# Kernel optimization log

Measured on AMD Instinct MI355X. Metric: run time of the kernel, lower is better.

Reference implementation:

```python
import jax, jax.numpy as jnp
import numpy as np

N_NODES = 50000
N_EDGES = 640000
D = 128
N_RELS = 16
N_NTYPES = 8


def setup_inputs() -> dict:
    key = jax.random.key(0)
    ks = jax.random.split(key, 9)
    return {
        "feats": jax.random.normal(ks[0], (N_NODES, D), dtype=jnp.float32),
        "W_edge": jax.random.normal(ks[1], (N_RELS, D, D), dtype=jnp.float32) / np.sqrt(D),
        "b_edge": jax.random.normal(ks[2], (N_RELS, D), dtype=jnp.float32) * 0.02,
        "W_node": jax.random.normal(ks[3], (N_NTYPES, D, D), dtype=jnp.float32) / np.sqrt(D),
        "b_node": jax.random.normal(ks[4], (N_NTYPES, D), dtype=jnp.float32) * 0.02,
        "src": jax.random.randint(ks[5], (N_EDGES,), 0, N_NODES, dtype=jnp.int32),
        "dst": jax.random.randint(ks[6], (N_EDGES,), 0, N_NODES, dtype=jnp.int32),
        "ntypes": jax.random.randint(ks[7], (N_NODES,), 0, N_NTYPES, dtype=jnp.int32),
        "etypes": jax.random.randint(ks[8], (N_EDGES,), 0, N_RELS, dtype=jnp.int32),
    }


def reference(feats, W_edge, b_edge, W_node, b_node, src, dst, ntypes, etypes):
    N, d = feats.shape
    T = W_edge.shape[0]
    # Per-relation linear applied to all nodes once: [T, N, out]; then gather per edge.
    hW = jnp.einsum('nd,tdf->tnf', feats, W_edge) + b_edge[:, None, :]
    msg = hW[etypes, src]  # [E, out]
    # Per-(dst-node, edge-type) in-degree counts (one_hot count normalization).
    seg = dst * T + etypes  # [E]
    counts = jax.ops.segment_sum(jnp.ones(msg.shape[0], dtype=msg.dtype), seg,
                                 num_segments=N * T)  # [N*T]
    msg = msg / counts[seg][:, None]
    # Scatter-sum messages into destination nodes (zero for isolated nodes).
    agg = jax.ops.segment_sum(msg, dst, num_segments=N)  # [N, out]
    # Type-conditional node transform + residual message + activation.
    hN = jnp.einsum('nd,tdf->tnf', feats, W_node) + b_node[:, None, :]  # [Tn, N, out]
    out = hN[ntypes, jnp.arange(N)] + agg
    return jax.nn.relu(out)
```

## Files before the change

### kernel.cpp

```cpp
#include <hip/hip_runtime.h>
#include <hip/hip_bf16.h>
#include <stdint.h>


#define D 128
#define TRELS 16
#define NTYPES 8

typedef __bf16 bf16x8 __attribute__((ext_vector_type(8)));
typedef float f32x4 __attribute__((ext_vector_type(4)));

__device__ __forceinline__ unsigned short f2bf(float f) {
  union { float f; unsigned u; } v; v.f = f;
  unsigned u = v.u;
  return (unsigned short)((u + 0x7FFFu + ((u >> 16) & 1u)) >> 16);
}
__device__ __forceinline__ float bf2f(unsigned short h) {
  union { unsigned u; float f; } v; v.u = ((unsigned)h) << 16;
  return v.f;
}

__global__ void prep_k(const float* __restrict__ feats,
                       const float* __restrict__ We,
                       const float* __restrict__ Wn,
                       unsigned short* __restrict__ featsbf,
                       unsigned short* __restrict__ WeT,
                       unsigned short* __restrict__ WnT,
                       int nfeat) {
  int idx = blockIdx.x * 256 + threadIdx.x;
  if (idx < nfeat) { featsbf[idx] = f2bf(feats[idx]); return; }
  idx -= nfeat;
  if (idx < TRELS * D * D) {
    int t = idx >> 14, rem = idx & 16383;
    int n = rem >> 7, k = rem & 127;
    WeT[idx] = f2bf(We[t * 16384 + k * 128 + n]);
    return;
  }
  idx -= TRELS * D * D;
  if (idx < NTYPES * D * D) {
    int t = idx >> 14, rem = idx & 16383;
    int n = rem >> 7, k = rem & 127;
    WnT[idx] = f2bf(Wn[t * 16384 + k * 128 + n]);
  }
}

__global__ void hist_k(const int* __restrict__ dst, const int* __restrict__ etypes,
                       const int* __restrict__ ntypes, int E, int N,
                       int* __restrict__ cnt, int* __restrict__ nhist) {
  __shared__ int sh_n[NTYPES];
  int tid = threadIdx.x;
  if (tid < NTYPES) sh_n[tid] = 0;
  __syncthreads();
  int g = blockIdx.x * 256 + tid;
  if (g < E) atomicAdd(&cnt[dst[g] * TRELS + etypes[g]], 1);
  if (g < N) atomicAdd(&sh_n[ntypes[g]], 1);
  __syncthreads();
  if (tid < NTYPES && sh_n[tid]) atomicAdd(&nhist[tid], sh_n[tid]);
}

__global__ void scan1_k(const int* __restrict__ cnt, int* __restrict__ doff,
                        int* __restrict__ bsum, int N) {
  __shared__ int sd[256];
  int b = blockIdx.x, tid = threadIdx.x;
  int base = b * 1024 + tid * 4;
  int v[4]; int tot = 0;
  for (int j = 0; j < 4; ++j) {
    int i = base + j;
    int dg = 0;
    if (i < N) {
      const int* row = cnt + i * TRELS;
#pragma unroll
      for (int et = 0; et < TRELS; ++et) dg += row[et];
    }
    v[j] = tot; tot += dg;
  }
  sd[tid] = tot;
  __syncthreads();
  for (int off = 1; off < 256; off <<= 1) {
    int t = (tid >= off) ? sd[tid - off] : 0;
    __syncthreads();
    sd[tid] += t;
    __syncthreads();
  }
  int excl = sd[tid] - tot;
  for (int j = 0; j < 4; ++j) {
    int i = base + j;
    if (i < N) doff[i] = excl + v[j];
  }
  if (tid == 255) bsum[b] = sd[255];
}

__global__ void scan2_k(int* __restrict__ misc, int* __restrict__ bsum, int nb) {
  if (threadIdx.x != 0) return;
  int run = 0;
  for (int b = 0; b < nb; ++b) { int t = bsum[b]; bsum[b] = run; run += t; }
  int* noff = misc; int* ntb = misc + 9; int* ncur = misc + 18; int* nhist = misc + 26;
  int s = 0, ts = 0;
  for (int t = 0; t < NTYPES; ++t) {
    noff[t] = s; ncur[t] = s; ntb[t] = ts;
    s += nhist[t]; ts += (nhist[t] + 127) >> 7;
  }
  noff[NTYPES] = s; ntb[NTYPES] = ts;
}

__global__ void scan3_k(int* __restrict__ doff, int* __restrict__ dcur,
                        const int* __restrict__ bsum, int N, int E) {
  int b = blockIdx.x, tid = threadIdx.x;
  int add = bsum[b];
  int base = b * 1024 + tid * 4;
  for (int j = 0; j < 4; ++j) {
    int i = base + j;
    if (i < N) { int o = doff[i] + add; doff[i] = o; dcur[i] = o; }
  }
  if (b == 0 && tid == 0) doff[N] = E;
}

__global__ void scatter_k(const int* __restrict__ src, const int* __restrict__ dst,
                          const int* __restrict__ etypes, const int* __restrict__ ntypes,
                          int E, int N, int* __restrict__ misc,
                          int* __restrict__ dcur,
                          int* __restrict__ edst, int* __restrict__ nsorted) {
  __shared__ int lc_n[NTYPES], lb_n[NTYPES];
  int tid = threadIdx.x;
  if (tid < NTYPES) lc_n[tid] = 0;
  __syncthreads();
  int g = blockIdx.x * 256 + tid;
  if (g < E) {
    int d = dst[g];
    int pos = atomicAdd(&dcur[d], 1);
    edst[pos] = src[g] * TRELS + etypes[g];
  }
  int tn = -1, idn = 0;
  if (g < N) { tn = ntypes[g]; idn = atomicAdd(&lc_n[tn], 1); }
  __syncthreads();
  if (tid < NTYPES && lc_n[tid]) lb_n[tid] = atomicAdd(&misc[18 + tid], lc_n[tid]);
  __syncthreads();
  if (g < N) nsorted[lb_n[tn] + idn] = g;
}

__global__ __launch_bounds__(256) void hw_gemm_k(
    const unsigned short* __restrict__ featsbf,
    const unsigned short* __restrict__ WeT,
    unsigned short* __restrict__ hW, int N) {
  __shared__ unsigned char Asm[128 * 264];
  int tid = threadIdx.x;
  int et = blockIdx.y;
  int tile = blockIdx.x;

  int lane = tid & 63, w = tid >> 6;
  int m = lane & 15, q = lane >> 4;
  int rw = (w & 1) * 64, cw = (w >> 1) * 64;

  const unsigned short* WB = WeT + et * (D * D);
  bf16x8 bfr[4][4];
#pragma unroll
  for (int ks = 0; ks < 4; ++ks)
#pragma unroll
    for (int j = 0; j < 4; ++j)
      bfr[ks][j] = *reinterpret_cast<const bf16x8*>(WB + (cw + j * 16 + m) * D + ks * 32 + q * 8);

  int r = tid >> 1, h = tid & 1;
  int row = tile * 128 + r;
  if (row < N) {
    const uint4* gp = reinterpret_cast<const uint4*>(featsbf + (size_t)row * D);
#pragma unroll
    for (int cc = 0; cc < 8; ++cc) {
      int c = h * 8 + cc;
      *reinterpret_cast<uint4*>(&Asm[r * 256 + ((c ^ (r & 7)) << 4)]) = gp[c];
    }
  }
  __syncthreads();

  f32x4 acc[4][4];
#pragma unroll
  for (int i = 0; i < 4; ++i)
#pragma unroll
    for (int j = 0; j < 4; ++j) acc[i][j] = (f32x4){0.f, 0.f, 0.f, 0.f};

#pragma unroll
  for (int ks = 0; ks < 4; ++ks) {
    bf16x8 a[4];
#pragma unroll
    for (int i = 0; i < 4; ++i) {
      int rr = rw + i * 16 + m;
      int c = ks * 4 + q;
      a[i] = *reinterpret_cast<const bf16x8*>(&Asm[rr * 256 + ((c ^ (rr & 7)) << 4)]);
    }
#pragma unroll
    for (int i = 0; i < 4; ++i)
#pragma unroll
      for (int j = 0; j < 4; ++j)
        acc[i][j] = __builtin_amdgcn_mfma_f32_16x16x32_bf16(a[i], bfr[ks][j], acc[i][j], 0, 0, 0);
  }

  __syncthreads();
  unsigned short* Cs = reinterpret_cast<unsigned short*>(Asm);
#pragma unroll
  for (int i = 0; i < 4; ++i)
#pragma unroll
    for (int j = 0; j < 4; ++j)
#pragma unroll
      for (int reg = 0; reg < 4; ++reg) {
        int rr = rw + i * 16 + q * 4 + reg;
        Cs[rr * 132 + cw + j * 16 + m] = f2bf(acc[i][j][reg]);
      }
  __syncthreads();
  char* gout = (char*)(hW + ((size_t)et * N + (size_t)tile * 128) * D);
#pragma unroll
  for (int cp = 0; cp < 8; ++cp) {
    int o = cp * 4096 + tid * 16;
    int rloc = o >> 8;
    if (tile * 128 + rloc < N) {
      uint4 v = *reinterpret_cast<const uint4*>(&Asm[rloc * 264 + (o & 255)]);
      *reinterpret_cast<uint4*>(gout + o) = v;
    }
  }
}

__global__ __launch_bounds__(256) void agg_k(
    const unsigned short* __restrict__ hW,
    const float* __restrict__ b_edge,
    const int* __restrict__ cnt,
    const int* __restrict__ doff, const int* __restrict__ edst,
    float* __restrict__ agg, int N) {
  int tid = threadIdx.x;
  int lane = tid & 63, w = tid >> 6;
  int d = blockIdx.x * 4 + w;
  if (d >= N) return;

  int cv = 0;
  if (lane < TRELS) cv = cnt[d * TRELS + lane];
  float invl = (cv > 0) ? 1.0f / (float)cv : 0.0f;

  int start = doff[d], end = doff[d + 1];
  float ax = 0.f, ay = 0.f;
  for (int base = start; base < end; base += 64) {
    int key = 0;
    if (base + lane < end) key = edst[base + lane];
    int nchunk = end - base; if (nchunk > 64) nchunk = 64;
    int j = 0;
    for (; j + 4 <= nchunk; j += 4) {
      int k0 = __shfl(key, j, 64), k1 = __shfl(key, j + 1, 64);
      int k2 = __shfl(key, j + 2, 64), k3 = __shfl(key, j + 3, 64);
      float i0 = __shfl(invl, k0 & 15, 64), i1 = __shfl(invl, k1 & 15, 64);
      float i2 = __shfl(invl, k2 & 15, 64), i3 = __shfl(invl, k3 & 15, 64);
      ushort2 h0 = *reinterpret_cast<const ushort2*>(hW + ((size_t)(k0 & 15) * N + (k0 >> 4)) * D + lane * 2);
      ushort2 h1 = *reinterpret_cast<const ushort2*>(hW + ((size_t)(k1 & 15) * N + (k1 >> 4)) * D + lane * 2);
      ushort2 h2 = *reinterpret_cast<const ushort2*>(hW + ((size_t)(k2 & 15) * N + (k2 >> 4)) * D + lane * 2);
      ushort2 h3 = *reinterpret_cast<const ushort2*>(hW + ((size_t)(k3 & 15) * N + (k3 >> 4)) * D + lane * 2);
      ax += i0 * bf2f(h0.x); ay += i0 * bf2f(h0.y);
      ax += i1 * bf2f(h1.x); ay += i1 * bf2f(h1.y);
      ax += i2 * bf2f(h2.x); ay += i2 * bf2f(h2.y);
      ax += i3 * bf2f(h3.x); ay += i3 * bf2f(h3.y);
    }
    for (; j < nchunk; ++j) {
      int k = __shfl(key, j, 64);
      float inv = __shfl(invl, k & 15, 64);
      ushort2 hv = *reinterpret_cast<const ushort2*>(hW + ((size_t)(k & 15) * N + (k >> 4)) * D + lane * 2);
      ax += inv * bf2f(hv.x); ay += inv * bf2f(hv.y);
    }
  }
#pragma unroll
  for (int et = 0; et < TRELS; ++et) {
    int c = __shfl(cv, et, 64);
    if (c > 0) {
      const float* bp = b_edge + et * D + lane * 2;
      ax += bp[0]; ay += bp[1];
    }
  }
  float2* op = reinterpret_cast<float2*>(agg + (size_t)d * D + lane * 2);
  *op = make_float2(ax, ay);
}

__global__ __launch_bounds__(256) void node_gemm_k(
    const unsigned short* __restrict__ featsbf,
    const unsigned short* __restrict__ WnT,
    const float* __restrict__ b_node,
    const int* __restrict__ nsorted, const int* __restrict__ misc,
    const float* __restrict__ agg,
    float* __restrict__ out) {
  __shared__ unsigned char Asm[128 * 264];
  __shared__ int sm_node[128];
  __shared__ int s_ntb[9];
  int tid = threadIdx.x;
  if (tid < 9) s_ntb[tid] = misc[9 + tid];
  __syncthreads();
  int bid = blockIdx.x;
  if (bid >= s_ntb[8]) return;
  int t = 0;
  while (bid >= s_ntb[t + 1]) ++t;
  int tile = bid - s_ntb[t];
  int noff_t = misc[t];
  int cntT = misc[t + 1] - noff_t;

  int lane = tid & 63, w = tid >> 6;
  int m = lane & 15, q = lane >> 4;
  int rw = (w & 1) * 64, cw = (w >> 1) * 64;

  const unsigned short* WB = WnT + t * (D * D);
  bf16x8 bfr[4][4];
#pragma unroll
  for (int ks = 0; ks < 4; ++ks)
#pragma unroll
    for (int j = 0; j < 4; ++j)
      bfr[ks][j] = *reinterpret_cast<const bf16x8*>(WB + (cw + j * 16 + m) * D + ks * 32 + q * 8);

  int r = tid >> 1, h = tid & 1;
  int gidx = tile * 128 + r;
  bool rv = gidx < cntT;
  int node = 0;
  if (rv) node = nsorted[noff_t + gidx];
  if (h == 0) sm_node[r] = rv ? node : -1;
  if (rv) {
    const uint4* gp = reinterpret_cast<const uint4*>(featsbf + (size_t)node * D);
#pragma unroll
    for (int cc = 0; cc < 8; ++cc) {
      int c = h * 8 + cc;
      *reinterpret_cast<uint4*>(&Asm[r * 256 + ((c ^ (r & 7)) << 4)]) = gp[c];
    }
  }
  __syncthreads();

  f32x4 acc[4][4];
#pragma unroll
  for (int i = 0; i < 4; ++i)
#pragma unroll
    for (int j = 0; j < 4; ++j) acc[i][j] = (f32x4){0.f, 0.f, 0.f, 0.f};

#pragma unroll
  for (int ks = 0; ks < 4; ++ks) {
    bf16x8 a[4];
#pragma unroll
    for (int i = 0; i < 4; ++i) {
      int rr = rw + i * 16 + m;
      int c = ks * 4 + q;
      a[i] = *reinterpret_cast<const bf16x8*>(&Asm[rr * 256 + ((c ^ (rr & 7)) << 4)]);
    }
#pragma unroll
    for (int i = 0; i < 4; ++i)
#pragma unroll
      for (int j = 0; j < 4; ++j)
        acc[i][j] = __builtin_amdgcn_mfma_f32_16x16x32_bf16(a[i], bfr[ks][j], acc[i][j], 0, 0, 0);
  }

  const float* bnp = b_node + t * D;
  float* Cf = reinterpret_cast<float*>(Asm);
  __syncthreads();
#pragma unroll
  for (int half = 0; half < 2; ++half) {
    if ((w & 1) == half) {
#pragma unroll
      for (int i = 0; i < 4; ++i)
#pragma unroll
        for (int j = 0; j < 4; ++j)
#pragma unroll
          for (int reg = 0; reg < 4; ++reg) {
            int rl = i * 16 + q * 4 + reg;
            Cf[rl * 132 + cw + j * 16 + m] = acc[i][j][reg];
          }
    }
    __syncthreads();
#pragma unroll
    for (int cp = 0; cp < 8; ++cp) {
      int o = cp * 4096 + tid * 16;
      int rl = o >> 9;
      int nd = sm_node[half * 64 + rl];
      if (nd >= 0) {
        int col = (o & 511) >> 2;
        f32x4 c = *reinterpret_cast<const f32x4*>((char*)Cf + rl * 528 + (o & 511));
        f32x4 a = *reinterpret_cast<const f32x4*>(agg + (size_t)nd * D + col);
        f32x4 b4 = *reinterpret_cast<const f32x4*>(bnp + col);
        f32x4 res;
#pragma unroll
        for (int z = 0; z < 4; ++z) res[z] = fmaxf(c[z] + a[z] + b4[z], 0.f);
        *reinterpret_cast<f32x4*>(out + (size_t)nd * D + col) = res;
      }
    }
    __syncthreads();
  }
}

static inline size_t align256(size_t x) { return (x + 255) & ~(size_t)255; }

extern "C" void kernel_launch(void* const* d_in, const int* in_sizes, int n_in,
                              void* d_out, int out_size, void* d_ws, size_t ws_size,
                              hipStream_t stream) {
  const float* feats  = (const float*)d_in[0];
  const float* W_edge = (const float*)d_in[1];
  const float* b_edge = (const float*)d_in[2];
  const float* W_node = (const float*)d_in[3];
  const float* b_node = (const float*)d_in[4];
  const int* src    = (const int*)d_in[5];
  const int* dst    = (const int*)d_in[6];
  const int* ntypes = (const int*)d_in[7];
  const int* etypes = (const int*)d_in[8];
  int N = in_sizes[0] / D;
  int E = in_sizes[5];

  char* ws = (char*)d_ws;
  size_t o_cnt  = 0;
  size_t o_misc = align256(o_cnt + (size_t)N * TRELS * 4);
  size_t zend   = align256(o_misc + 512);
  size_t o_doff = zend;
  size_t o_dcur = align256(o_doff + (size_t)(N + 1) * 4);
  size_t o_edst = align256(o_dcur + (size_t)N * 4);
  size_t o_ns   = align256(o_edst + (size_t)E * 4);
  size_t o_fb   = align256(o_ns + (size_t)N * 4);
  size_t o_we   = align256(o_fb + (size_t)N * D * 2);
  size_t o_wn   = align256(o_we + (size_t)TRELS * D * D * 2);
  size_t o_agg  = align256(o_wn + (size_t)NTYPES * D * D * 2);
  size_t o_hw   = align256(o_agg + (size_t)N * D * 4);

  int* cnt = (int*)(ws + o_cnt);
  int* misc = (int*)(ws + o_misc);
  int* doff = (int*)(ws + o_doff);
  int* dcur = (int*)(ws + o_dcur);
  int* edst = (int*)(ws + o_edst);
  int* nsorted = (int*)(ws + o_ns);
  unsigned short* featsbf = (unsigned short*)(ws + o_fb);
  unsigned short* WeT = (unsigned short*)(ws + o_we);
  unsigned short* WnT = (unsigned short*)(ws + o_wn);
  float* agg = (float*)(ws + o_agg);
  unsigned short* hW = (unsigned short*)(ws + o_hw);
  int* bsum = misc + 64;

  hipMemsetAsync(ws, 0, zend, stream);

  int nfeat = N * D;
  int ptot = nfeat + TRELS * D * D + NTYPES * D * D;
  prep_k<<<(ptot + 255) / 256, 256, 0, stream>>>(feats, W_edge, W_node, featsbf, WeT, WnT, nfeat);

  int hgrid = ((E > N ? E : N) + 255) / 256;
  hist_k<<<hgrid, 256, 0, stream>>>(dst, etypes, ntypes, E, N, cnt, misc + 26);

  int nb = (N + 1023) / 1024;
  scan1_k<<<nb, 256, 0, stream>>>(cnt, doff, bsum, N);
  scan2_k<<<1, 64, 0, stream>>>(misc, bsum, nb);
  scan3_k<<<nb, 256, 0, stream>>>(doff, dcur, bsum, N, E);

  scatter_k<<<hgrid, 256, 0, stream>>>(src, dst, etypes, ntypes, E, N, misc, dcur, edst, nsorted);

  int mtiles = (N + 127) / 128;
  dim3 ggrid(mtiles, TRELS);
  hw_gemm_k<<<ggrid, 256, 0, stream>>>(featsbf, WeT, hW, N);

  agg_k<<<(N + 3) / 4, 256, 0, stream>>>(hW, b_edge, cnt, doff, edst, agg, N);

  int ngrid = mtiles + NTYPES;
  node_gemm_k<<<ngrid, 256, 0, stream>>>(featsbf, WnT, b_node, nsorted, misc, agg, (float*)d_out);
}
```

Measured before the change: 339.3 us.

## Skip writing unreferenced hW rows and reuse feature tile across four relations

The scatter pass now marks each (src, relation) pair that some edge actually references. The relation GEMM writes back only the marked rows of hW, which cuts global store traffic, since roughly half the rows are never gathered. Each block also loops over four relations, so the staged feature tile is reused and the grid shrinks fourfold. The cost is an extra byte-mask memset and scattered byte writes, plus fewer blocks in flight and more syncs per block.

```diff
diff --git a/kernel.cpp b/kernel.cpp
--- a/kernel.cpp
+++ b/kernel.cpp
@@ -119,7 +119,8 @@
                           const int* __restrict__ etypes, const int* __restrict__ ntypes,
                           int E, int N, int* __restrict__ misc,
                           int* __restrict__ dcur,
-                          int* __restrict__ edst, int* __restrict__ nsorted) {
+                          int* __restrict__ edst, unsigned char* __restrict__ mark,
+                          int* __restrict__ nsorted) {
   __shared__ int lc_n[NTYPES], lb_n[NTYPES];
   int tid = threadIdx.x;
   if (tid < NTYPES) lc_n[tid] = 0;
@@ -127,8 +128,10 @@
   int g = blockIdx.x * 256 + tid;
   if (g < E) {
     int d = dst[g];
+    int key = src[g] * TRELS + etypes[g];
     int pos = atomicAdd(&dcur[d], 1);
-    edst[pos] = src[g] * TRELS + etypes[g];
+    edst[pos] = key;
+    mark[key] = 1;
   }
   int tn = -1, idn = 0;
   if (g < N) { tn = ntypes[g]; idn = atomicAdd(&lc_n[tn], 1); }
@@ -141,23 +144,18 @@
 __global__ __launch_bounds__(256) void hw_gemm_k(
     const unsigned short* __restrict__ featsbf,
     const unsigned short* __restrict__ WeT,
+    const unsigned char* __restrict__ mark,
     unsigned short* __restrict__ hW, int N) {
-  __shared__ unsigned char Asm[128 * 264];
+  __shared__ unsigned char Asm[128 * 256];
+  __shared__ unsigned char Csm[64 * 264];
+  __shared__ unsigned char sm_mask[128];
   int tid = threadIdx.x;
-  int et = blockIdx.y;
   int tile = blockIdx.x;
+  int etg = blockIdx.y;
 
   int lane = tid & 63, w = tid >> 6;
   int m = lane & 15, q = lane >> 4;
   int rw = (w & 1) * 64, cw = (w >> 1) * 64;
-
-  const unsigned short* WB = WeT + et * (D * D);
-  bf16x8 bfr[4][4];
-#pragma unroll
-  for (int ks = 0; ks < 4; ++ks)
-#pragma unroll
-    for (int j = 0; j < 4; ++j)
-      bfr[ks][j] = *reinterpret_cast<const bf16x8*>(WB + (cw + j * 16 + m) * D + ks * 32 + q * 8);
 
   int r = tid >> 1, h = tid & 1;
   int row = tile * 128 + r;
@@ -171,48 +169,70 @@
   }
   __syncthreads();
 
-  f32x4 acc[4][4];
-#pragma unroll
-  for (int i = 0; i < 4; ++i)
-#pragma unroll
-    for (int j = 0; j < 4; ++j) acc[i][j] = (f32x4){0.f, 0.f, 0.f, 0.f};
-
-#pragma unroll
-  for (int ks = 0; ks < 4; ++ks) {
-    bf16x8 a[4];
-#pragma unroll
-    for (int i = 0; i < 4; ++i) {
-      int rr = rw + i * 16 + m;
-      int c = ks * 4 + q;
-      a[i] = *reinterpret_cast<const bf16x8*>(&Asm[rr * 256 + ((c ^ (rr & 7)) << 4)]);
-    }
+  for (int ee = 0; ee < 4; ++ee) {
+    int et = etg * 4 + ee;
+    const unsigned short* WB = WeT + et * (D * D);
+    bf16x8 bfr[4][4];
+#pragma unroll
+    for (int ks = 0; ks < 4; ++ks)
+#pragma unroll
+      for (int j = 0; j < 4; ++j)
+        bfr[ks][j] = *reinterpret_cast<const bf16x8*>(WB + (cw + j * 16 + m) * D + ks * 32 + q * 8);
+
+    f32x4 acc[4][4];
 #pragma unroll
     for (int i = 0; i < 4; ++i)
 #pragma unroll
-      for (int j = 0; j < 4; ++j)
-        acc[i][j] = __builtin_amdgcn_mfma_f32_16x16x32_bf16(a[i], bfr[ks][j], acc[i][j], 0, 0, 0);
-  }
-
-  __syncthreads();
-  unsigned short* Cs = reinterpret_cast<unsigned short*>(Asm);
-#pragma unroll
-  for (int i = 0; i < 4; ++i)
-#pragma unroll
-    for (int j = 0; j < 4; ++j)
-#pragma unroll
-      for (int reg = 0; reg < 4; ++reg) {
-        int rr = rw + i * 16 + q * 4 + reg;
-        Cs[rr * 132 + cw + j * 16 + m] = f2bf(acc[i][j][reg]);
+      for (int j = 0; j < 4; ++j) acc[i][j] = (f32x4){0.f, 0.f, 0.f, 0.f};
+
+#pragma unroll
+    for (int ks = 0; ks < 4; ++ks) {
+      bf16x8 a[4];
+#pragma unroll
+      for (int i = 0; i < 4; ++i) {
+        int rr = rw + i * 16 + m;
+        int c = ks * 4 + q;
+        a[i] = *reinterpret_cast<const bf16x8*>(&Asm[rr * 256 + ((c ^ (rr & 7)) << 4)]);
       }
-  __syncthreads();
-  char* gout = (char*)(hW + ((size_t)et * N + (size_t)tile * 128) * D);
-#pragma unroll
-  for (int cp = 0; cp < 8; ++cp) {
-    int o = cp * 4096 + tid * 16;
-    int rloc = o >> 8;
-    if (tile * 128 + rloc < N) {
-      uint4 v = *reinterpret_cast<const uint4*>(&Asm[rloc * 264 + (o & 255)]);
-      *reinterpret_cast<uint4*>(gout + o) = v;
+#pragma unroll
+      for (int i = 0; i < 4; ++i)
+#pragma unroll
+        for (int j = 0; j < 4; ++j)
+          acc[i][j] = __builtin_amdgcn_mfma_f32_16x16x32_bf16(a[i], bfr[ks][j], acc[i][j], 0, 0, 0);
+    }
+
+    unsigned short* Cs = reinterpret_cast<unsigned short*>(Csm);
+    char* gout = (char*)(hW + ((size_t)et * N + (size_t)tile * 128) * D);
+    __syncthreads();
+    if (tid < 128) {
+      int gr = tile * 128 + tid;
+      sm_mask[tid] = (gr < N) ? mark[(size_t)gr * TRELS + et] : 0;
+    }
+#pragma unroll
+    for (int half = 0; half < 2; ++half) {
+      if (half) __syncthreads();
+      if ((w & 1) == half) {
+#pragma unroll
+        for (int i = 0; i < 4; ++i)
+#pragma unroll
+          for (int j = 0; j < 4; ++j)
+#pragma unroll
+            for (int reg = 0; reg < 4; ++reg) {
+              int rl = i * 16 + q * 4 + reg;
+              Cs[rl * 132 + cw + j * 16 + m] = f2bf(acc[i][j][reg]);
+            }
+      }
+      __syncthreads();
+#pragma unroll
+      for (int cp = 0; cp < 4; ++cp) {
+        int o = cp * 4096 + tid * 16;
+        int rl = o >> 8;
+        int grow = tile * 128 + half * 64 + rl;
+        if (grow < N && sm_mask[half * 64 + rl]) {
+          uint4 v = *reinterpret_cast<const uint4*>(&Csm[rl * 264 + (o & 255)]);
+          *reinterpret_cast<uint4*>(gout + half * 16384 + o) = v;
+        }
+      }
     }
   }
 }
@@ -400,7 +420,8 @@
   char* ws = (char*)d_ws;
   size_t o_cnt  = 0;
   size_t o_misc = align256(o_cnt + (size_t)N * TRELS * 4);
-  size_t zend   = align256(o_misc + 512);
+  size_t o_mark = align256(o_misc + 512);
+  size_t zend   = align256(o_mark + (size_t)N * TRELS);
   size_t o_doff = zend;
   size_t o_dcur = align256(o_doff + (size_t)(N + 1) * 4);
   size_t o_edst = align256(o_dcur + (size_t)N * 4);
@@ -413,6 +434,7 @@
 
   int* cnt = (int*)(ws + o_cnt);
   int* misc = (int*)(ws + o_misc);
+  unsigned char* mark = (unsigned char*)(ws + o_mark);
   int* doff = (int*)(ws + o_doff);
   int* dcur = (int*)(ws + o_dcur);
   int* edst = (int*)(ws + o_edst);
@@ -438,11 +460,11 @@
   scan2_k<<<1, 64, 0, stream>>>(misc, bsum, nb);
   scan3_k<<<nb, 256, 0, stream>>>(doff, dcur, bsum, N, E);
 
-  scatter_k<<<hgrid, 256, 0, stream>>>(src, dst, etypes, ntypes, E, N, misc, dcur, edst, nsorted);
+  scatter_k<<<hgrid, 256, 0, stream>>>(src, dst, etypes, ntypes, E, N, misc, dcur, edst, mark, nsorted);
 
   int mtiles = (N + 127) / 128;
-  dim3 ggrid(mtiles, TRELS);
-  hw_gemm_k<<<ggrid, 256, 0, stream>>>(featsbf, WeT, hW, N);
+  dim3 ggrid(mtiles, 4);
+  hw_gemm_k<<<ggrid, 256, 0, stream>>>(featsbf, WeT, mark, hW, N);
 
   agg_k<<<(N + 3) / 4, 256, 0, stream>>>(hW, b_edge, cnt, doff, edst, agg, N);
 
```

Result: slower. 351.5 us (+3.6%).
